# Kernel optimization log

Measured on AMD Instinct MI355X. Metric: run time of the kernel, lower is better.

## Reference

```python
import jax, jax.numpy as jnp
import numpy as np


def setup_inputs() -> dict:
    key = jax.random.key(0)
    k = jax.random.split(key, 5)
    B, L, D = 8, 2048, 256  # D = 2*d_model, c_len == q_len == L (required by source's s1 broadcast)
    c = jax.random.normal(k[0], (B, L, D), dtype=jnp.float32)
    q = jax.random.normal(k[1], (B, L, D), dtype=jnp.float32)
    c_weight = jax.random.normal(k[2], (D, 1), dtype=jnp.float32) * 0.05
    q_weight = jax.random.normal(k[3], (D, 1), dtype=jnp.float32) * 0.05
    cq_weight = jax.random.normal(k[4], (1, 1, D), dtype=jnp.float32) * 0.05
    bias = jnp.zeros((1,), dtype=jnp.float32)
    return {"c": c, "q": q, "c_weight": c_weight, "q_weight": q_weight,
            "cq_weight": cq_weight, "bias": bias}


def reference(c, q, c_weight, q_weight, cq_weight, bias):
    # Dropout omitted (identity) for a deterministic reference.
    # s0: [B, c_len, 1] -> broadcasts over q_len
    s0 = jnp.matmul(c, c_weight)                       # [B, L, 1]
    # s1 (faithful to source, which uses c here): [B, 1, c_len]
    s1 = jnp.swapaxes(jnp.matmul(c, q_weight), 1, 2)   # [B, 1, L]
    # s2: elementwise-scaled batched GEMM: [B, c_len, q_len]
    s2 = jnp.matmul(c * cq_weight, jnp.swapaxes(q, 1, 2))
    s = s0 + s1 + s2 + bias                            # broadcast sum + scalar bias
    return s
```

## Files before the change

### kernel.cpp

```cpp
#include <hip/hip_runtime.h>
#include <hip/hip_bf16.h>

#define B_ 8
#define L_ 2048
#define D_ 256

typedef __bf16 bf16x8 __attribute__((ext_vector_type(8)));
typedef float f32x4 __attribute__((ext_vector_type(4)));

static __device__ __forceinline__ unsigned short f2bf(float f) {
    unsigned int u = __builtin_bit_cast(unsigned int, f);
    unsigned int lsb = (u >> 16) & 1u;
    u += 0x7fffu + lsb;
    return (unsigned short)(u >> 16);
}

static __device__ __forceinline__ void gload_lds16(const void* g, void* l) {
    __builtin_amdgcn_global_load_lds(
        (const __attribute__((address_space(1))) unsigned int*)g,
        (__attribute__((address_space(3))) unsigned int*)l, 16, 0, 0);
}

__global__ __launch_bounds__(256) void prep_kernel(
    const float* __restrict__ c, const float* __restrict__ q,
    const float* __restrict__ cw, const float* __restrict__ qw,
    const float* __restrict__ cqw, const float* __restrict__ bias,
    unsigned short* __restrict__ Abf, unsigned short* __restrict__ Qbf,
    float* __restrict__ s0, float* __restrict__ s1)
{
    const int wave = threadIdx.x >> 6;
    const int lane = threadIdx.x & 63;
    const int row  = blockIdx.x * 4 + wave;

    const float4 cv  = *(const float4*)(c   + (size_t)row * D_ + lane * 4);
    const float4 qv  = *(const float4*)(q   + (size_t)row * D_ + lane * 4);
    const float4 wc  = *(const float4*)(cw  + lane * 4);
    const float4 wq  = *(const float4*)(qw  + lane * 4);
    const float4 wcq = *(const float4*)(cqw + lane * 4);

    ushort4 av, qb;
    av.x = f2bf(cv.x * wcq.x); av.y = f2bf(cv.y * wcq.y);
    av.z = f2bf(cv.z * wcq.z); av.w = f2bf(cv.w * wcq.w);
    qb.x = f2bf(qv.x); qb.y = f2bf(qv.y);
    qb.z = f2bf(qv.z); qb.w = f2bf(qv.w);
    *(ushort4*)(Abf + (size_t)row * D_ + lane * 4) = av;
    *(ushort4*)(Qbf + (size_t)row * D_ + lane * 4) = qb;

    float p0 = cv.x * wc.x + cv.y * wc.y + cv.z * wc.z + cv.w * wc.w;
    float p1 = cv.x * wq.x + cv.y * wq.y + cv.z * wq.z + cv.w * wq.w;
    #pragma unroll
    for (int off = 32; off > 0; off >>= 1) {
        p0 += __shfl_down(p0, off);
        p1 += __shfl_down(p1, off);
    }
    if (lane == 0) { s0[row] = p0 + bias[0]; s1[row] = p1; }
}

#define BM 128
#define BN 128
#define BK 64

__global__ __launch_bounds__(256) void gemm_kernel(
    const unsigned short* __restrict__ A, const unsigned short* __restrict__ Q,
    const float* __restrict__ s0, const float* __restrict__ s1,
    float* __restrict__ out)
{
    __shared__ __align__(16) unsigned short As[BM * BK];
    __shared__ __align__(16) unsigned short Qs[BN * BK];

    const int tid  = threadIdx.x;
    const int wave = tid >> 6;
    const int lane = tid & 63;

    const int lin = blockIdx.x + (blockIdx.y << 4) + (blockIdx.z << 8);
    const int nl  = ((lin & 7) << 8) | (lin >> 3);
    const int b   = nl >> 8;
    const int brow = ((nl >> 4) & 15) * BM;
    const int bcol = (nl & 15) * BN;

    const unsigned short* Ab = A + ((size_t)b * L_ + brow) * D_;
    const unsigned short* Qb = Q + ((size_t)b * L_ + bcol) * D_;

    const int wr = wave >> 1;
    const int wc = wave & 1;

    const f32x4 zero = {0.f, 0.f, 0.f, 0.f};
    f32x4 acc[4][4];
    #pragma unroll
    for (int m = 0; m < 4; ++m)
        #pragma unroll
        for (int n = 0; n < 4; ++n) acc[m][n] = zero;

    const int srow_in = lane >> 3;
    const int sslot   = lane & 7;

    for (int kt = 0; kt < D_ / BK; ++kt) {
        const int k0 = kt * BK;
        #pragma unroll
        for (int cc = 0; cc < 4; ++cc) {
            const int chunk = wave * 4 + cc;
            const int row   = chunk * 8 + srow_in;
            const int swz   = sslot ^ (row & 7);
            gload_lds16(Ab + (size_t)row * D_ + k0 + swz * 8, As + chunk * 512);
            gload_lds16(Qb + (size_t)row * D_ + k0 + swz * 8, Qs + chunk * 512);
        }
        __syncthreads();

        #pragma unroll
        for (int kk = 0; kk < 2; ++kk) {
            bf16x8 af[4], qf[4];
            #pragma unroll
            for (int m = 0; m < 4; ++m) {
                const int row  = wr * 64 + m * 16 + (lane & 15);
                const int byte = row * 128 +
                    ((kk * 64 + (lane >> 4) * 16) ^ ((row & 7) << 4));
                af[m] = *(const bf16x8*)((const char*)As + byte);
            }
            #pragma unroll
            for (int n = 0; n < 4; ++n) {
                const int row  = wc * 64 + n * 16 + (lane & 15);
                const int byte = row * 128 +
                    ((kk * 64 + (lane >> 4) * 16) ^ ((row & 7) << 4));
                qf[n] = *(const bf16x8*)((const char*)Qs + byte);
            }
            #pragma unroll
            for (int m = 0; m < 4; ++m)
                #pragma unroll
                for (int n = 0; n < 4; ++n)
                    acc[m][n] = __builtin_amdgcn_mfma_f32_16x16x32_bf16(
                        af[m], qf[n], acc[m][n], 0, 0, 0);
        }
        __syncthreads();
    }

    const float* s0b = s0 + b * L_ + brow;
    const float* s1b = s1 + b * L_ + bcol;
    float s1v[4];
    #pragma unroll
    for (int n = 0; n < 4; ++n) s1v[n] = s1b[wc * 64 + n * 16 + (lane & 15)];
    float* outb = out + ((size_t)b * L_ + brow) * L_ + bcol;
    #pragma unroll
    for (int m = 0; m < 4; ++m) {
        #pragma unroll
        for (int r = 0; r < 4; ++r) {
            const int i = wr * 64 + m * 16 + (lane >> 4) * 4 + r;
            const float s0v = s0b[i];
            float* orow = outb + (size_t)i * L_;
            #pragma unroll
            for (int n = 0; n < 4; ++n)
                __builtin_nontemporal_store(acc[m][n][r] + s0v + s1v[n],
                    &orow[wc * 64 + n * 16 + (lane & 15)]);
        }
    }
}

__global__ void naive_kernel(const float* __restrict__ c, const float* __restrict__ q,
                             const float* __restrict__ cw, const float* __restrict__ qw,
                             const float* __restrict__ cqw, const float* __restrict__ bias,
                             float* __restrict__ out)
{
    const size_t total = (size_t)B_ * L_ * L_;
    for (size_t idx = (size_t)blockIdx.x * blockDim.x + threadIdx.x; idx < total;
         idx += (size_t)gridDim.x * blockDim.x) {
        const int b = (int)(idx / ((size_t)L_ * L_));
        const int rem = (int)(idx % ((size_t)L_ * L_));
        const int i = rem / L_, j = rem % L_;
        const float* ci = c + ((size_t)b * L_ + i) * D_;
        const float* cj = c + ((size_t)b * L_ + j) * D_;
        const float* qj = q + ((size_t)b * L_ + j) * D_;
        float acc = bias[0];
        for (int d = 0; d < D_; ++d)
            acc += ci[d] * cw[d] + cj[d] * qw[d] + ci[d] * cqw[d] * qj[d];
        out[idx] = acc;
    }
}

extern "C" void kernel_launch(void* const* d_in, const int* in_sizes, int n_in,
                              void* d_out, int out_size, void* d_ws, size_t ws_size,
                              hipStream_t stream) {
    const float* c    = (const float*)d_in[0];
    const float* q    = (const float*)d_in[1];
    const float* cw   = (const float*)d_in[2];
    const float* qw   = (const float*)d_in[3];
    const float* cqw  = (const float*)d_in[4];
    const float* bias = (const float*)d_in[5];
    float* out = (float*)d_out;

    const size_t bytesA = (size_t)B_ * L_ * D_ * 2;
    const size_t need   = 2 * bytesA + 2 * (size_t)B_ * L_ * 4;

    if (ws_size >= need) {
        unsigned short* Abf = (unsigned short*)d_ws;
        unsigned short* Qbf = (unsigned short*)((char*)d_ws + bytesA);
        float* s0 = (float*)((char*)d_ws + 2 * bytesA);
        float* s1 = s0 + (size_t)B_ * L_;
        prep_kernel<<<B_ * L_ / 4, 256, 0, stream>>>(c, q, cw, qw, cqw, bias,
                                                     Abf, Qbf, s0, s1);
        dim3 grid(L_ / BN, L_ / BM, B_);
        gemm_kernel<<<grid, 256, 0, stream>>>(Abf, Qbf, s0, s1, out);
    } else {
        naive_kernel<<<2048, 256, 0, stream>>>(c, q, cw, qw, cqw, bias, out);
    }
}
```

Measured before the change: 52.84 us.

## Triple-buffer GEMM K-loop with BK=32 and explicit vmcnt waits

```diff
diff --git a/kernel.cpp b/kernel.cpp
--- a/kernel.cpp
+++ b/kernel.cpp
@@ -58,15 +58,16 @@
 
 #define BM 128
 #define BN 128
-#define BK 64
+#define BK 32
+#define NSTEP (D_ / BK)
 
 __global__ __launch_bounds__(256) void gemm_kernel(
     const unsigned short* __restrict__ A, const unsigned short* __restrict__ Q,
     const float* __restrict__ s0, const float* __restrict__ s1,
     float* __restrict__ out)
 {
-    __shared__ __align__(16) unsigned short As[BM * BK];
-    __shared__ __align__(16) unsigned short Qs[BN * BK];
+    __shared__ __align__(16) unsigned short As[3][BM * BK];
+    __shared__ __align__(16) unsigned short Qs[3][BM * BK];
 
     const int tid  = threadIdx.x;
     const int wave = tid >> 6;
@@ -91,47 +92,65 @@
         #pragma unroll
         for (int n = 0; n < 4; ++n) acc[m][n] = zero;
 
-    const int srow_in = lane >> 3;
-    const int sslot   = lane & 7;
-
-    for (int kt = 0; kt < D_ / BK; ++kt) {
-        const int k0 = kt * BK;
-        #pragma unroll
-        for (int cc = 0; cc < 4; ++cc) {
-            const int chunk = wave * 4 + cc;
-            const int row   = chunk * 8 + srow_in;
-            const int swz   = sslot ^ (row & 7);
-            gload_lds16(Ab + (size_t)row * D_ + k0 + swz * 8, As + chunk * 512);
-            gload_lds16(Qb + (size_t)row * D_ + k0 + swz * 8, Qs + chunk * 512);
-        }
-        __syncthreads();
-
-        #pragma unroll
-        for (int kk = 0; kk < 2; ++kk) {
-            bf16x8 af[4], qf[4];
+    auto stage = [&](int s) {
+        const int k0 = s * BK;
+        unsigned short* ab = &As[s % 3][0];
+        unsigned short* qb = &Qs[s % 3][0];
+        #pragma unroll
+        for (int i = 0; i < 2; ++i) {
+            const int sidx = i * 256 + wave * 64 + lane;
+            const int row  = sidx >> 2;
+            const int sl   = sidx & 3;
+            const int ksrc = k0 + ((sl ^ ((row >> 1) & 3)) << 3);
+            const int wbase = (i * 256 + wave * 64) * 8;
+            gload_lds16(Ab + (size_t)row * D_ + ksrc, ab + wbase);
+            gload_lds16(Qb + (size_t)row * D_ + ksrc, qb + wbase);
+        }
+    };
+
+    auto compute = [&](int t) {
+        const unsigned short* ab = &As[t % 3][0];
+        const unsigned short* qb = &Qs[t % 3][0];
+        bf16x8 af[4], qf[4];
+        #pragma unroll
+        for (int m = 0; m < 4; ++m) {
+            const int row = wr * 64 + m * 16 + (lane & 15);
+            const int idx = row * 32 + (((lane >> 4) ^ ((row >> 1) & 3)) << 3);
+            af[m] = *(const bf16x8*)(ab + idx);
+        }
+        #pragma unroll
+        for (int n = 0; n < 4; ++n) {
+            const int row = wc * 64 + n * 16 + (lane & 15);
+            const int idx = row * 32 + (((lane >> 4) ^ ((row >> 1) & 3)) << 3);
+            qf[n] = *(const bf16x8*)(qb + idx);
+        }
+        __builtin_amdgcn_s_setprio(1);
+        #pragma unroll
+        for (int m = 0; m < 4; ++m)
             #pragma unroll
-            for (int m = 0; m < 4; ++m) {
-                const int row  = wr * 64 + m * 16 + (lane & 15);
-                const int byte = row * 128 +
-                    ((kk * 64 + (lane >> 4) * 16) ^ ((row & 7) << 4));
-                af[m] = *(const bf16x8*)((const char*)As + byte);
-            }
-            #pragma unroll
-            for (int n = 0; n < 4; ++n) {
-                const int row  = wc * 64 + n * 16 + (lane & 15);
-                const int byte = row * 128 +
-                    ((kk * 64 + (lane >> 4) * 16) ^ ((row & 7) << 4));
-                qf[n] = *(const bf16x8*)((const char*)Qs + byte);
-            }
-            #pragma unroll
-            for (int m = 0; m < 4; ++m)
-                #pragma unroll
-                for (int n = 0; n < 4; ++n)
-                    acc[m][n] = __builtin_amdgcn_mfma_f32_16x16x32_bf16(
-                        af[m], qf[n], acc[m][n], 0, 0, 0);
-        }
-        __syncthreads();
-    }
+            for (int n = 0; n < 4; ++n)
+                acc[m][n] = __builtin_amdgcn_mfma_f32_16x16x32_bf16(
+                    af[m], qf[n], acc[m][n], 0, 0, 0);
+        __builtin_amdgcn_s_setprio(0);
+    };
+
+    stage(0);
+    stage(1);
+
+#define STEP(T, VM) do {                                        \
+        if ((T) + 2 < NSTEP) stage((T) + 2);                    \
+        asm volatile("s_waitcnt vmcnt(" #VM ")" ::: "memory");  \
+        __builtin_amdgcn_s_barrier();                           \
+        asm volatile("" ::: "memory");                          \
+        compute(T);                                             \
+        asm volatile("" ::: "memory");                          \
+        __builtin_amdgcn_s_barrier();                           \
+        asm volatile("" ::: "memory");                          \
+    } while (0)
+
+    STEP(0, 8); STEP(1, 8); STEP(2, 8); STEP(3, 8);
+    STEP(4, 8); STEP(5, 8); STEP(6, 4); STEP(7, 0);
+#undef STEP
 
     const float* s0b = s0 + b * L_ + brow;
     const float* s1b = s1 + b * L_ + bcol;
@@ -148,8 +167,7 @@
             float* orow = outb + (size_t)i * L_;
             #pragma unroll
             for (int n = 0; n < 4; ++n)
-                __builtin_nontemporal_store(acc[m][n][r] + s0v + s1v[n],
-                    &orow[wc * 64 + n * 16 + (lane & 15)]);
+                orow[wc * 64 + n * 16 + (lane & 15)] = acc[m][n][r] + s0v + s1v[n];
         }
     }
 }
```

Measured after the change: 47.45 us. 1.11x faster.

## Pipeline GEMM with triple-buffered LDS and overlap output stores across column tiles

Applied to the files above, without the earlier changes.

```diff
diff --git a/kernel.cpp b/kernel.cpp
--- a/kernel.cpp
+++ b/kernel.cpp
@@ -58,100 +58,164 @@
 
 #define BM 128
 #define BN 128
-#define BK 64
-
-__global__ __launch_bounds__(256) void gemm_kernel(
+#define BK 32
+
+__global__ __launch_bounds__(256, 2) void gemm_kernel(
     const unsigned short* __restrict__ A, const unsigned short* __restrict__ Q,
     const float* __restrict__ s0, const float* __restrict__ s1,
     float* __restrict__ out)
 {
-    __shared__ __align__(16) unsigned short As[BM * BK];
-    __shared__ __align__(16) unsigned short Qs[BN * BK];
+    __shared__ __align__(16) unsigned short As[3][BM * BK];
+    __shared__ __align__(16) unsigned short Qs[3][BM * BK];
 
     const int tid  = threadIdx.x;
     const int wave = tid >> 6;
     const int lane = tid & 63;
 
-    const int lin = blockIdx.x + (blockIdx.y << 4) + (blockIdx.z << 8);
-    const int nl  = ((lin & 7) << 8) | (lin >> 3);
-    const int b   = nl >> 8;
-    const int brow = ((nl >> 4) & 15) * BM;
-    const int bcol = (nl & 15) * BN;
+    const int beta = blockIdx.x;
+    const int bs   = ((beta & 7) << 6) | (beta >> 3);
+    const int b    = bs >> 6;
+    const int rpnl = (bs >> 2) & 15;
+    const int cg   = bs & 3;
+    const int brow  = rpnl * BM;
+    const int bcol0 = cg * 4 * BN;
 
     const unsigned short* Ab = A + ((size_t)b * L_ + brow) * D_;
-    const unsigned short* Qb = Q + ((size_t)b * L_ + bcol) * D_;
+    const unsigned short* Qb = Q + ((size_t)b * L_ + bcol0) * D_;
+    float* outp = out + ((size_t)b * L_ + brow) * L_ + bcol0;
 
     const int wr = wave >> 1;
     const int wc = wave & 1;
 
-    const f32x4 zero = {0.f, 0.f, 0.f, 0.f};
-    f32x4 acc[4][4];
+    float s0v[4][4];
     #pragma unroll
     for (int m = 0; m < 4; ++m)
         #pragma unroll
-        for (int n = 0; n < 4; ++n) acc[m][n] = zero;
-
-    const int srow_in = lane >> 3;
-    const int sslot   = lane & 7;
-
-    for (int kt = 0; kt < D_ / BK; ++kt) {
-        const int k0 = kt * BK;
-        #pragma unroll
-        for (int cc = 0; cc < 4; ++cc) {
-            const int chunk = wave * 4 + cc;
-            const int row   = chunk * 8 + srow_in;
-            const int swz   = sslot ^ (row & 7);
-            gload_lds16(Ab + (size_t)row * D_ + k0 + swz * 8, As + chunk * 512);
-            gload_lds16(Qb + (size_t)row * D_ + k0 + swz * 8, Qs + chunk * 512);
-        }
-        __syncthreads();
-
-        #pragma unroll
-        for (int kk = 0; kk < 2; ++kk) {
-            bf16x8 af[4], qf[4];
+        for (int r = 0; r < 4; ++r)
+            s0v[m][r] = s0[(size_t)b * L_ + brow + wr * 64 + m * 16 + (lane >> 4) * 4 + r];
+    float s1v[4][4];
+    #pragma unroll
+    for (int t = 0; t < 4; ++t)
+        #pragma unroll
+        for (int n = 0; n < 4; ++n)
+            s1v[t][n] = s1[(size_t)b * L_ + bcol0 + t * BN + wc * 64 + n * 16 + (lane & 15)];
+
+    f32x4 acc[4][4], st[4][4];
+    #pragma unroll
+    for (int m = 0; m < 4; ++m)
+        #pragma unroll
+        for (int n = 0; n < 4; ++n)
             #pragma unroll
-            for (int m = 0; m < 4; ++m) {
-                const int row  = wr * 64 + m * 16 + (lane & 15);
-                const int byte = row * 128 +
-                    ((kk * 64 + (lane >> 4) * 16) ^ ((row & 7) << 4));
-                af[m] = *(const bf16x8*)((const char*)As + byte);
-            }
-            #pragma unroll
-            for (int n = 0; n < 4; ++n) {
-                const int row  = wc * 64 + n * 16 + (lane & 15);
-                const int byte = row * 128 +
-                    ((kk * 64 + (lane >> 4) * 16) ^ ((row & 7) << 4));
-                qf[n] = *(const bf16x8*)((const char*)Qs + byte);
-            }
-            #pragma unroll
-            for (int m = 0; m < 4; ++m)
-                #pragma unroll
-                for (int n = 0; n < 4; ++n)
-                    acc[m][n] = __builtin_amdgcn_mfma_f32_16x16x32_bf16(
-                        af[m], qf[n], acc[m][n], 0, 0, 0);
-        }
-        __syncthreads();
-    }
-
-    const float* s0b = s0 + b * L_ + brow;
-    const float* s1b = s1 + b * L_ + bcol;
-    float s1v[4];
-    #pragma unroll
-    for (int n = 0; n < 4; ++n) s1v[n] = s1b[wc * 64 + n * 16 + (lane & 15)];
-    float* outb = out + ((size_t)b * L_ + brow) * L_ + bcol;
-    #pragma unroll
-    for (int m = 0; m < 4; ++m) {
+            for (int r = 0; r < 4; ++r)
+                acc[m][n][r] = s0v[m][r] + s1v[0][n];
+
+#define STAGE(G) do {                                                        \
+        const int k0_ = ((G) & 7) * BK;                                      \
+        const size_t qo_ = (size_t)((G) >> 3) * BN * D_;                     \
+        unsigned short* ab_ = &As[(G) % 3][0];                               \
+        unsigned short* qb_ = &Qs[(G) % 3][0];                               \
+        _Pragma("unroll")                                                    \
+        for (int i_ = 0; i_ < 2; ++i_) {                                     \
+            const int sidx_ = i_ * 256 + wave * 64 + lane;                   \
+            const int row_  = sidx_ >> 2;                                    \
+            const int sl_   = sidx_ & 3;                                     \
+            const int ks_   = k0_ + ((sl_ ^ ((row_ >> 1) & 3)) << 3);        \
+            const int wb_   = (i_ * 256 + wave * 64) * 8;                    \
+            gload_lds16(Ab + (size_t)row_ * D_ + ks_, ab_ + wb_);            \
+            gload_lds16(Qb + qo_ + (size_t)row_ * D_ + ks_, qb_ + wb_);      \
+        }                                                                    \
+    } while (0)
+
+#define COMPUTE(G) do {                                                      \
+        const unsigned short* ab_ = &As[(G) % 3][0];                         \
+        const unsigned short* qb_ = &Qs[(G) % 3][0];                         \
+        bf16x8 af_[4], qf_[4];                                               \
+        _Pragma("unroll")                                                    \
+        for (int m_ = 0; m_ < 4; ++m_) {                                     \
+            const int row_ = wr * 64 + m_ * 16 + (lane & 15);                \
+            const int idx_ = row_ * 32 + (((lane >> 4) ^ ((row_ >> 1) & 3)) << 3); \
+            af_[m_] = *(const bf16x8*)(ab_ + idx_);                          \
+        }                                                                    \
+        _Pragma("unroll")                                                    \
+        for (int n_ = 0; n_ < 4; ++n_) {                                     \
+            const int row_ = wc * 64 + n_ * 16 + (lane & 15);                \
+            const int idx_ = row_ * 32 + (((lane >> 4) ^ ((row_ >> 1) & 3)) << 3); \
+            qf_[n_] = *(const bf16x8*)(qb_ + idx_);                          \
+        }                                                                    \
+        __builtin_amdgcn_s_setprio(1);                                       \
+        _Pragma("unroll")                                                    \
+        for (int m_ = 0; m_ < 4; ++m_)                                       \
+            _Pragma("unroll")                                                \
+            for (int n_ = 0; n_ < 4; ++n_)                                   \
+                acc[m_][n_] = __builtin_amdgcn_mfma_f32_16x16x32_bf16(       \
+                    af_[m_], qf_[n_], acc[m_][n_], 0, 0, 0);                 \
+        __builtin_amdgcn_s_setprio(0);                                       \
+    } while (0)
+
+#define SLICE(G) do { if ((G) >= 8) {                                        \
+        const int t_ = ((G) >> 3) - 1, s_ = (G) & 7, m_ = s_ >> 1;           \
+        _Pragma("unroll")                                                    \
+        for (int rr_ = 0; rr_ < 2; ++rr_) {                                  \
+            const int r_   = (s_ & 1) * 2 + rr_;                             \
+            const int row_ = wr * 64 + m_ * 16 + (lane >> 4) * 4 + r_;       \
+            float* rp_ = outp + (size_t)t_ * BN + (size_t)row_ * L_;         \
+            _Pragma("unroll")                                                \
+            for (int n_ = 0; n_ < 4; ++n_)                                   \
+                rp_[wc * 64 + n_ * 16 + (lane & 15)] = st[m_][n_][r_];       \
+        } } } while (0)
+
+#define BOUNDARY(G) do { if (((G) & 7) == 7 && (G) < 31) {                   \
+        const int tn_ = ((G) >> 3) + 1;                                      \
+        _Pragma("unroll")                                                    \
+        for (int m_ = 0; m_ < 4; ++m_)                                       \
+            _Pragma("unroll")                                                \
+            for (int n_ = 0; n_ < 4; ++n_) {                                 \
+                st[m_][n_] = acc[m_][n_];                                    \
+                _Pragma("unroll")                                            \
+                for (int r_ = 0; r_ < 4; ++r_)                               \
+                    acc[m_][n_][r_] = s0v[m_][r_] + s1v[tn_][n_];            \
+            }                                                                \
+    } } while (0)
+
+#define STEP(G, VM) do {                                                     \
+        if ((G) + 2 < 32) STAGE((G) + 2);                                    \
+        SLICE(G);                                                            \
+        asm volatile("s_waitcnt vmcnt(" #VM ")" ::: "memory");               \
+        __builtin_amdgcn_s_barrier();                                        \
+        COMPUTE(G);                                                          \
+        asm volatile("" ::: "memory");                                       \
+        __builtin_amdgcn_s_barrier();                                        \
+        BOUNDARY(G);                                                         \
+    } while (0)
+
+    STAGE(0); STAGE(1);
+
+    STEP(0, 8);   STEP(1, 8);   STEP(2, 8);   STEP(3, 8);
+    STEP(4, 8);   STEP(5, 8);   STEP(6, 8);   STEP(7, 8);
+    STEP(8, 16);  STEP(9, 24);
+    STEP(10, 32); STEP(11, 32); STEP(12, 32); STEP(13, 32);
+    STEP(14, 32); STEP(15, 32); STEP(16, 32); STEP(17, 32);
+    STEP(18, 32); STEP(19, 32); STEP(20, 32); STEP(21, 32);
+    STEP(22, 32); STEP(23, 32); STEP(24, 32); STEP(25, 32);
+    STEP(26, 32); STEP(27, 32); STEP(28, 32); STEP(29, 32);
+    STEP(30, 28); STEP(31, 24);
+
+#undef STEP
+#undef BOUNDARY
+#undef SLICE
+#undef COMPUTE
+#undef STAGE
+
+    #pragma unroll
+    for (int m = 0; m < 4; ++m)
         #pragma unroll
         for (int r = 0; r < 4; ++r) {
-            const int i = wr * 64 + m * 16 + (lane >> 4) * 4 + r;
-            const float s0v = s0b[i];
-            float* orow = outb + (size_t)i * L_;
+            const int row = wr * 64 + m * 16 + (lane >> 4) * 4 + r;
+            float* rp = outp + (size_t)3 * BN + (size_t)row * L_;
             #pragma unroll
             for (int n = 0; n < 4; ++n)
-                __builtin_nontemporal_store(acc[m][n][r] + s0v + s1v[n],
-                    &orow[wc * 64 + n * 16 + (lane & 15)]);
+                rp[wc * 64 + n * 16 + (lane & 15)] = acc[m][n][r];
         }
-    }
 }
 
 __global__ void naive_kernel(const float* __restrict__ c, const float* __restrict__ q,
@@ -196,8 +260,7 @@
         float* s1 = s0 + (size_t)B_ * L_;
         prep_kernel<<<B_ * L_ / 4, 256, 0, stream>>>(c, q, cw, qw, cqw, bias,
                                                      Abf, Qbf, s0, s1);
-        dim3 grid(L_ / BN, L_ / BM, B_);
-        gemm_kernel<<<grid, 256, 0, stream>>>(Abf, Qbf, s0, s1, out);
+        gemm_kernel<<<dim3(512), 256, 0, stream>>>(Abf, Qbf, s0, s1, out);
     } else {
         naive_kernel<<<2048, 256, 0, stream>>>(c, q, cw, qw, cqw, bias, out);
     }
```

Result: faster. 51.09 us (-3.3%).
